# Optimization experiments

Hardware: AMD Instinct MI355X
Metric: run time of the kernel (lower is better)

The kernel has to match this reference:

```python
import jax, jax.numpy as jnp
import numpy as np

BLKQ = 128   # query block size (BLOCK_M)
BLKK = 64    # key block size (BLOCK_N)
TOPK_RATIO = 0.1
EPS = 1e-5


def _block_mean(x, blk):
    # x: (B,H,L,D) -> (B,H,L//blk,D) mean over each block (compress_kernel)
    B, H, L, D = x.shape
    return x.reshape(B, H, L // blk, blk, D).mean(axis=3)


def setup_inputs() -> dict:
    key = jax.random.key(0)
    ks = jax.random.split(key, 5)
    B, L, H, D = 2, 4096, 16, 64
    return {
        "query": jax.random.normal(ks[0], (B, L, H, D), dtype=jnp.float32),
        "key":   jax.random.normal(ks[1], (B, L, H, D), dtype=jnp.float32),
        "value": jax.random.normal(ks[2], (B, L, H, D), dtype=jnp.float32),
        "W": 0.02 * jax.random.normal(ks[3], (D, D), dtype=jnp.float32),
        "b": 0.02 * jax.random.normal(ks[4], (D,), dtype=jnp.float32),
    }


def reference(query, key, value, W, b):
    # inputs (B,L,H,D) -> internal (B,H,L,D)
    q = jnp.transpose(query, (0, 2, 1, 3))
    k = jnp.transpose(key, (0, 2, 1, 3))
    v = jnp.transpose(value, (0, 2, 1, 3))
    B, H, L, D = q.shape
    scale = D ** (-0.5)

    # ---- get_block_map: mean-pooled block scoring + top-k LUT ----
    arg_k = k - k.mean(axis=2, keepdims=True)
    pq = _block_mean(q, BLKQ)        # (B,H,M,D)
    pk = _block_mean(arg_k, BLKK)    # (B,H,KB,D)
    score = jnp.einsum('bhmd,bhkd->bhmk', pq, pk)  # (B,H,M,KB)
    KB = score.shape[-1]
    topk = min(KB, int(TOPK_RATIO * KB))
    _, lut = jax.lax.top_k(score, topk)            # (B,H,M,topk) int32

    # ---- block-sparse attention over gathered K/V blocks ----
    M = L // BLKQ
    kb = k.reshape(B, H, KB, BLKK, D)
    vb = v.reshape(B, H, KB, BLKK, D)
    idx = lut.reshape(B, H, M * topk, 1, 1)
    gk = jnp.take_along_axis(kb, idx, axis=2).reshape(B, H, M, topk * BLKK, D)
    gv = jnp.take_along_axis(vb, idx, axis=2).reshape(B, H, M, topk * BLKK, D)
    qb = q.reshape(B, H, M, BLKQ, D)
    logits = jnp.einsum('bhmqd,bhmnd->bhmqn', qb, gk) * scale
    p = jax.nn.softmax(logits, axis=-1)  # online softmax over union of selected blocks
    o_s = jnp.einsum('bhmqn,bhmnd->bhmqd', p, gv).reshape(B, H, L, D)

    # ---- linear attention branch (feature_map='softmax') ----
    qf = jax.nn.softmax(q, axis=-1)
    kf = jax.nn.softmax(k, axis=-1)
    kv = jnp.einsum('bhld,bhle->bhde', kf, v)
    num = jnp.einsum('bhld,bhde->bhle', qf, kv)
    den = jnp.einsum('bhld,bhd->bhl', qf, kf.sum(axis=2))
    o_l = num / (EPS + den[..., None])
    o_l = jnp.einsum('bhld,ed->bhle', o_l, W) + b  # proj_l

    out = jnp.transpose(o_s + o_l, (0, 2, 1, 3))  # back to (B,L,H,D)
    return out
```

## Files before the change

kernel.cpp:

```cpp
#include <hip/hip_runtime.h>
#include <math.h>
#include <cstdint>
#include <cstddef>

#define B_    2
#define LSEQ  4096
#define H_    16
#define D_    64
#define M_    32
#define KB_   64
#define TOPK  6
#define SCALE 0.125f
#define LOG2E 1.4426950408889634f
#define SCL2  (SCALE * LOG2E)
#define EPSL  1e-5f
#define SPLIT 32
#define PSTR  65

typedef __attribute__((ext_vector_type(8))) short short8;
typedef __attribute__((ext_vector_type(4))) float f32x4;

#define LGKM_FENCE()   __asm__ volatile("s_waitcnt lgkmcnt(0)" ::: "memory")
#define BLOCK_BARRIER() __asm__ volatile("s_waitcnt lgkmcnt(0)\n\ts_barrier" ::: "memory")

__device__ __forceinline__ short bf16_rne(float x) {
  unsigned u = __float_as_uint(x);
  return (short)((u + 0x7fffu + ((u >> 16) & 1u)) >> 16);
}
__device__ __forceinline__ unsigned pack2_rne(float a, float b) {
  return ((unsigned)(unsigned short)bf16_rne(a)) | (((unsigned)(unsigned short)bf16_rne(b)) << 16);
}
__device__ __forceinline__ float bf16_to_f32(short s) {
  return __uint_as_float(((unsigned)(unsigned short)s) << 16);
}

__global__ __launch_bounds__(256) void lin_stats_kernel(
    const float* __restrict__ kin, const float* __restrict__ vin,
    const float* __restrict__ qin,
    float* __restrict__ kv, float* __restrict__ kfs,
    float* __restrict__ pkw, float* __restrict__ pqw)
{
  int blk   = blockIdx.x;
  int chunk = blk & (SPLIT - 1);
  int bh    = blk / SPLIT;
  int h = bh & (H_ - 1);
  int b = bh >> 4;
  int tid = threadIdx.x;
  int w = tid >> 6, lane = tid & 63, quad = lane >> 4, l15 = lane & 15;

  __shared__ __align__(16) float kraw[64 * 68];
  __shared__ __align__(16) short sA[64 * 64];
  __shared__ __align__(16) short sB[80 * 64];
  __shared__ float pred[512];

  for (int i = tid; i < 1024; i += 256) {
    int row = 64 + (i >> 6);
    sB[row * 64 + (i & 63)] = (row == 64) ? (short)0x3F80 : (short)0;
  }

  {
    int c4 = tid & 15, r0 = tid >> 4;
    float4 s = {0.f, 0.f, 0.f, 0.f};
    for (int i = 0; i < 8; i++) {
      int row = r0 + i * 16;
      float4 x = *(const float4*)(qin + (((size_t)b * LSEQ + chunk * 128 + row) * H_ + h) * D_ + c4 * 4);
      s.x += x.x; s.y += x.y; s.z += x.z; s.w += x.w;
    }
    ((float4*)kraw)[tid] = s;
    BLOCK_BARRIER();
    if (tid < 16) {
      float4 a = {0.f, 0.f, 0.f, 0.f};
      for (int j = 0; j < 16; j++) {
        float4 x = ((float4*)kraw)[j * 16 + tid];
        a.x += x.x; a.y += x.y; a.z += x.z; a.w += x.w;
      }
      float4 o = {a.x * (1.f/128.f), a.y * (1.f/128.f), a.z * (1.f/128.f), a.w * (1.f/128.f)};
      *(float4*)(pqw + ((size_t)bh * 32 + chunk) * 64 + tid * 4) = o;
    }
  }

  f32x4 acc[5];
#pragma unroll
  for (int nt = 0; nt < 5; nt++) acc[nt] = (f32x4){0.f, 0.f, 0.f, 0.f};

  for (int t2 = 0; t2 < 2; ++t2) {
    int kbs = chunk * 2 + t2;
    int l0  = chunk * 128 + t2 * 64;
    BLOCK_BARRIER();
#pragma unroll
    for (int i = 0; i < 4; i++) {
      int f = tid + i * 256;
      int row = f >> 4, c4 = f & 15;
      *(float4*)(kraw + row * 68 + c4 * 4) =
        *(const float4*)(kin + (((size_t)b * LSEQ + l0 + row) * H_ + h) * D_ + c4 * 4);
    }
    {
      const float* vp = vin + (((size_t)b * LSEQ + l0 + lane) * H_ + h) * D_ + w * 16;
      float4 a0 = *(const float4*)(vp + 0);
      float4 a1 = *(const float4*)(vp + 4);
      float4 a2 = *(const float4*)(vp + 8);
      float4 a3 = *(const float4*)(vp + 12);
      float f[16] = {a0.x,a0.y,a0.z,a0.w, a1.x,a1.y,a1.z,a1.w,
                     a2.x,a2.y,a2.z,a2.w, a3.x,a3.y,a3.z,a3.w};
#pragma unroll
      for (int j = 0; j < 16; j++) {
        int e = w * 16 + j;
        int col = (((lane >> 3) ^ (e & 7)) << 3) | (lane & 7);
        sB[e * 64 + col] = bf16_rne(f[j]);
      }
    }
    BLOCK_BARRIER();
    {
      float kp = 0.f;
#pragma unroll
      for (int i = 0; i < 16; i++) kp += kraw[(w * 16 + i) * 68 + lane];
      pred[256 + w * 64 + lane] = kp;
    }
    float kr[16];
    *(float4*)(kr + 0)  = *(const float4*)(kraw + lane * 68 + w * 16 + 0);
    *(float4*)(kr + 4)  = *(const float4*)(kraw + lane * 68 + w * 16 + 4);
    *(float4*)(kr + 8)  = *(const float4*)(kraw + lane * 68 + w * 16 + 8);
    *(float4*)(kr + 12) = *(const float4*)(kraw + lane * 68 + w * 16 + 12);
    float ps = 0.f;
#pragma unroll
    for (int j = 0; j < 16; j++) { kr[j] = __expf(kr[j]); ps += kr[j]; }
    pred[w * 64 + lane] = ps;
    BLOCK_BARRIER();
    float ssum = pred[lane] + pred[64 + lane] + pred[128 + lane] + pred[192 + lane];
    float scl = 1.f / ssum;
    if (tid < 64) {
      float s = pred[256 + tid] + pred[320 + tid] + pred[384 + tid] + pred[448 + tid];
      pkw[((size_t)bh * 64 + kbs) * 64 + tid] = s * (1.f / 64.f);
    }
#pragma unroll
    for (int j = 0; j < 16; j++) {
      int d = w * 16 + j;
      int col = (((lane >> 3) ^ (d & 7)) << 3) | (lane & 7);
      sA[d * 64 + col] = bf16_rne(kr[j] * scl);
    }
    BLOCK_BARRIER();
    short8 af[2];
#pragma unroll
    for (int ks = 0; ks < 2; ks++) {
      int row = w * 16 + l15;
      int bi = (ks * 4 + quad) ^ (row & 7);
      af[ks] = *(const short8*)(sA + row * 64 + bi * 8);
    }
#pragma unroll
    for (int nt = 0; nt < 5; nt++) {
      int row = nt * 16 + l15;
#pragma unroll
      for (int ks = 0; ks < 2; ks++) {
        int bi = (ks * 4 + quad) ^ (row & 7);
        short8 bf = *(const short8*)(sB + row * 64 + bi * 8);
        acc[nt] = __builtin_amdgcn_mfma_f32_16x16x32_bf16(af[ks], bf, acc[nt], 0, 0, 0);
      }
    }
  }
  size_t kvb = (size_t)bh * 4096;
  int d0 = w * 16 + quad * 4;
#pragma unroll
  for (int nt = 0; nt < 4; nt++)
#pragma unroll
    for (int r = 0; r < 4; r++)
      atomicAdd(&kv[kvb + (size_t)(d0 + r) * 64 + nt * 16 + l15], acc[nt][r]);
  if (l15 == 0) {
#pragma unroll
    for (int r = 0; r < 4; r++)
      atomicAdd(&kfs[bh * 64 + d0 + r], acc[4][r]);
  }
}

__global__ __launch_bounds__(256) void blockmap_kernel(
    const float* __restrict__ pkw, const float* __restrict__ pqw,
    int* __restrict__ lut)
{
  int bh = blockIdx.x;
  int tid = threadIdx.x;

  __shared__ float pk[64 * PSTR];
  __shared__ float pq[32 * PSTR];
  __shared__ float sc[32 * PSTR];
  __shared__ float km[64];

#pragma unroll
  for (int i = 0; i < 16; i++) {
    int o = tid + i * 256;
    pk[(o >> 6) * PSTR + (o & 63)] = pkw[(size_t)bh * 4096 + o];
  }
#pragma unroll
  for (int i = 0; i < 8; i++) {
    int o = tid + i * 256;
    pq[(o >> 6) * PSTR + (o & 63)] = pqw[(size_t)bh * 2048 + o];
  }
  __syncthreads();
  if (tid < 64) {
    float s = 0.f;
#pragma unroll
    for (int kb = 0; kb < 64; kb++) s += pk[kb * PSTR + tid];
    km[tid] = s * (1.f / 64.f);
  }
  __syncthreads();
#pragma unroll
  for (int i = 0; i < 16; i++) {
    int o = tid + i * 256;
    int kb = o >> 6, d = o & 63;
    pk[kb * PSTR + d] -= km[d];
  }
  __syncthreads();
#pragma unroll
  for (int i = 0; i < 8; i++) {
    int o = tid + i * 256;
    int mb = o >> 6, kb = o & 63;
    float s = 0.f;
#pragma unroll
    for (int d = 0; d < 64; d++) s += pq[mb * PSTR + d] * pk[kb * PSTR + d];
    sc[mb * PSTR + kb] = s;
  }
  __syncthreads();
  if (tid < 32) {
    float* row = sc + tid * PSTR;
    int lb = (bh * M_ + tid) * TOPK;
    for (int s = 0; s < TOPK; s++) {
      float best = -INFINITY; int bi = 0;
      for (int j = 0; j < 64; j++) {
        float v = row[j];
        if (v > best) { best = v; bi = j; }
      }
      lut[lb + s] = bi;
      row[bi] = -INFINITY;
    }
  }
}

__global__ __launch_bounds__(256, 3) void sparse_attn_kernel(
    const float* __restrict__ qin, const float* __restrict__ kin,
    const float* __restrict__ vin, const int* __restrict__ lut,
    const float* __restrict__ kv, const float* __restrict__ kfs,
    const float* __restrict__ Wg, const float* __restrict__ biasg,
    float* __restrict__ out)
{
  int blk = blockIdx.x;
  int x = blk & 7, g = blk >> 3;
  int bh = x * 4 + (g & 3);
  int m  = g >> 2;
  int h = bh & (H_ - 1);
  int b = bh >> 4;
  int t = threadIdx.x;
  int w = t >> 6, lane = t & 63, quad = lane >> 4, l15 = lane & 15;

  __shared__ __align__(16) char smem[37120];
  short* sK  = (short*)smem;
  short* sV  = (short*)(smem + 8192);
  short* sP  = (short*)(smem + 18432);
  short* skv  = (short*)(smem + 18432);
  short* sW   = (short*)(smem + 28672);
  float* sbias= (float*)(smem + 36864);
  short* wPs = sP + w * 1024;
  short* olS = (short*)smem + w * 1024;

  for (int i = t; i < 1024; i += 256) {
    int row = 64 + (i >> 6);
    sV[row * 64 + (i & 63)] = (row == 64) ? (short)0x3F80 : (short)0;
  }

  short8 qA[2][2];
#pragma unroll
  for (int mt = 0; mt < 2; mt++) {
    int qrow = m * 128 + w * 32 + mt * 16 + l15;
    const float* qp = qin + (((size_t)b * LSEQ + qrow) * H_ + h) * D_;
#pragma unroll
    for (int ks = 0; ks < 2; ks++) {
      int d0 = ks * 32 + quad * 8;
      float4 a0 = *(const float4*)(qp + d0);
      float4 a1 = *(const float4*)(qp + d0 + 4);
      union { int4 i; short8 s; } u;
      u.i.x = pack2_rne(a0.x * SCL2, a0.y * SCL2);
      u.i.y = pack2_rne(a0.z * SCL2, a0.w * SCL2);
      u.i.z = pack2_rne(a1.x * SCL2, a1.y * SCL2);
      u.i.w = pack2_rne(a1.z * SCL2, a1.w * SCL2);
      qA[mt][ks] = u.s;
    }
  }

  f32x4 O[2][4];
  f32x4 Lacc[2];
#pragma unroll
  for (int mt = 0; mt < 2; mt++) {
#pragma unroll
    for (int dt = 0; dt < 4; dt++) O[mt][dt] = (f32x4){0.f, 0.f, 0.f, 0.f};
    Lacc[mt] = (f32x4){0.f, 0.f, 0.f, 0.f};
  }

  int lbase = (bh * M_ + m) * TOPK;
  int kbs_[TOPK];
#pragma unroll
  for (int i = 0; i < TOPK; i++) kbs_[i] = lut[lbase + i];

  float4 pk0, pk1, pk2, pk3;
  float4 pv0, pv1, pv2, pv3;
  const int kkey = t >> 2, kc = t & 3;
  const int vkey = t & 63;

  {
    int kb = kbs_[0];
    const float* kp = kin + (((size_t)b * LSEQ + (size_t)kb * 64 + kkey) * H_ + h) * D_ + kc * 16;
    pk0 = *(const float4*)(kp + 0);  pk1 = *(const float4*)(kp + 4);
    pk2 = *(const float4*)(kp + 8);  pk3 = *(const float4*)(kp + 12);
    const float* vp = vin + (((size_t)b * LSEQ + (size_t)kb * 64 + vkey) * H_ + h) * D_ + w * 16;
    pv0 = *(const float4*)(vp + 0);  pv1 = *(const float4*)(vp + 4);
    pv2 = *(const float4*)(vp + 8);  pv3 = *(const float4*)(vp + 12);
  }

  for (int s = 0; s < TOPK; s++) {
    BLOCK_BARRIER();
    {
      int4 h0, h1;
      h0.x = pack2_rne(pk0.x, pk0.y);  h0.y = pack2_rne(pk0.z, pk0.w);
      h0.z = pack2_rne(pk1.x, pk1.y);  h0.w = pack2_rne(pk1.z, pk1.w);
      h1.x = pack2_rne(pk2.x, pk2.y);  h1.y = pack2_rne(pk2.z, pk2.w);
      h1.z = pack2_rne(pk3.x, pk3.y);  h1.w = pack2_rne(pk3.z, pk3.w);
      int base = kkey * 64;
      int b0 = ((kc * 2    ) ^ (kkey & 7)) << 3;
      int b1 = ((kc * 2 + 1) ^ (kkey & 7)) << 3;
      *(int4*)(sK + base + b0) = h0;
      *(int4*)(sK + base + b1) = h1;
    }
    {
      float f[16] = {pv0.x,pv0.y,pv0.z,pv0.w, pv1.x,pv1.y,pv1.z,pv1.w,
                     pv2.x,pv2.y,pv2.z,pv2.w, pv3.x,pv3.y,pv3.z,pv3.w};
#pragma unroll
      for (int j = 0; j < 16; j++) {
        int d = w * 16 + j;
        int col = (((vkey >> 3) ^ (d & 7)) << 3) | (vkey & 7);
        sV[d * 64 + col] = bf16_rne(f[j]);
      }
    }
    BLOCK_BARRIER();
    if (s + 1 < TOPK) {
      int kb = kbs_[s + 1];
      const float* kp = kin + (((size_t)b * LSEQ + (size_t)kb * 64 + kkey) * H_ + h) * D_ + kc * 16;
      pk0 = *(const float4*)(kp + 0);  pk1 = *(const float4*)(kp + 4);
      pk2 = *(const float4*)(kp + 8);  pk3 = *(const float4*)(kp + 12);
      const float* vp = vin + (((size_t)b * LSEQ + (size_t)kb * 64 + vkey) * H_ + h) * D_ + w * 16;
      pv0 = *(const float4*)(vp + 0);  pv1 = *(const float4*)(vp + 4);
      pv2 = *(const float4*)(vp + 8);  pv3 = *(const float4*)(vp + 12);
    }

#pragma unroll
    for (int mt = 0; mt < 2; mt++) {
      f32x4 S[4];
#pragma unroll
      for (int nt = 0; nt < 4; nt++) {
        f32x4 acc = (f32x4){0.f, 0.f, 0.f, 0.f};
        int row = nt * 16 + l15;
#pragma unroll
        for (int ks = 0; ks < 2; ks++) {
          int blk8 = ((ks * 4 + quad) ^ (row & 7)) << 3;
          short8 kh = *(const short8*)(sK + row * 64 + blk8);
          acc = __builtin_amdgcn_mfma_f32_16x16x32_bf16(qA[mt][ks], kh, acc, 0, 0, 0);
        }
        S[nt] = acc;
      }
#pragma unroll
      for (int r = 0; r < 4; r++) {
        int prow = quad * 4 + r;
#pragma unroll
        for (int nt = 0; nt < 4; nt++) {
          int key = nt * 16 + l15;
          int idx = prow * 64 + ((((key >> 3) ^ (prow & 7)) << 3) | (key & 7));
          wPs[idx] = bf16_rne(__builtin_amdgcn_exp2f(S[nt][r]));
        }
      }
      LGKM_FENCE();
      short8 pA[2];
#pragma unroll
      for (int ks = 0; ks < 2; ks++) {
        int blk8 = ((ks * 4 + quad) ^ (l15 & 7)) << 3;
        pA[ks] = *(const short8*)(wPs + l15 * 64 + blk8);
      }
      LGKM_FENCE();
#pragma unroll
      for (int dt = 0; dt < 5; dt++) {
        f32x4 acc = (dt < 4) ? O[mt][dt] : Lacc[mt];
        int row = dt * 16 + l15;
#pragma unroll
        for (int ks = 0; ks < 2; ks++) {
          int blk8 = ((ks * 4 + quad) ^ (row & 7)) << 3;
          short8 vh = *(const short8*)(sV + row * 64 + blk8);
          acc = __builtin_amdgcn_mfma_f32_16x16x32_bf16(pA[ks], vh, acc, 0, 0, 0);
        }
        if (dt < 4) O[mt][dt] = acc; else Lacc[mt] = acc;
      }
    }
  }

#pragma unroll
  for (int mt = 0; mt < 2; mt++)
#pragma unroll
    for (int r = 0; r < 4; r++) {
      float lv = __shfl(Lacc[mt][r], lane & 48);
      float inv = 1.f / lv;
#pragma unroll
      for (int dt = 0; dt < 4; dt++) O[mt][dt][r] *= inv;
    }

  BLOCK_BARRIER();
#pragma unroll
  for (int i = 0; i < 16; i++) {
    int idx = t + i * 256;
    int d = idx >> 6, e = idx & 63;
    int c1 = (((d >> 3) ^ (e & 7)) << 3) | (d & 7);
    skv[e * 64 + c1] = bf16_rne(kv[(size_t)bh * 4096 + idx]);
    int eo = idx >> 6, dd = idx & 63;
    int c2 = (((dd >> 3) ^ (eo & 7)) << 3) | (dd & 7);
    sW[eo * 64 + c2] = bf16_rne(Wg[idx]);
  }
#pragma unroll
  for (int j = 0; j < 4; j++) {
    int idx2 = t + j * 256;
    int row = 64 + (idx2 >> 6), col = idx2 & 63;
    skv[row * 64 + col] = (row == 64) ? bf16_rne(kfs[bh * 64 + col]) : (short)0;
  }
  if (t < 64) sbias[t] = biasg[t];
  BLOCK_BARRIER();

  const short8 onesB = {(short)0x3F80,(short)0x3F80,(short)0x3F80,(short)0x3F80,
                        (short)0x3F80,(short)0x3F80,(short)0x3F80,(short)0x3F80};

#pragma unroll
  for (int mt = 0; mt < 2; mt++) {
    float eq[2][8];
    short8 eqs[2];
#pragma unroll
    for (int ks = 0; ks < 2; ks++) {
      union { short8 s; short a[8]; } uu; uu.s = qA[mt][ks];
      union { int4 i; short8 s; } pp;
      unsigned pw[4];
#pragma unroll
      for (int j = 0; j < 8; j++)
        eq[ks][j] = __builtin_amdgcn_exp2f(8.f * bf16_to_f32(uu.a[j]));
#pragma unroll
      for (int j2 = 0; j2 < 4; j2++)
        pw[j2] = pack2_rne(eq[ks][j2 * 2], eq[ks][j2 * 2 + 1]);
      pp.i.x = (int)pw[0]; pp.i.y = (int)pw[1]; pp.i.z = (int)pw[2]; pp.i.w = (int)pw[3];
      eqs[ks] = pp.s;
    }
    f32x4 ssv = (f32x4){0.f, 0.f, 0.f, 0.f};
    ssv = __builtin_amdgcn_mfma_f32_16x16x32_bf16(eqs[0], onesB, ssv, 0, 0, 0);
    ssv = __builtin_amdgcn_mfma_f32_16x16x32_bf16(eqs[1], onesB, ssv, 0, 0, 0);
    int srcl = (l15 >> 2) << 4;
    float s0 = __shfl(ssv[0], srcl);
    float s1 = __shfl(ssv[1], srcl);
    float s2 = __shfl(ssv[2], srcl);
    float s3 = __shfl(ssv[3], srcl);
    int rr = l15 & 3;
    float ssrow = (rr == 0) ? s0 : (rr == 1) ? s1 : (rr == 2) ? s2 : s3;
    float qinv = 1.f / ssrow;
    short8 qf[2];
#pragma unroll
    for (int ks = 0; ks < 2; ks++) {
      union { int4 i; short8 s; } pp;
      pp.i.x = (int)pack2_rne(eq[ks][0] * qinv, eq[ks][1] * qinv);
      pp.i.y = (int)pack2_rne(eq[ks][2] * qinv, eq[ks][3] * qinv);
      pp.i.z = (int)pack2_rne(eq[ks][4] * qinv, eq[ks][5] * qinv);
      pp.i.w = (int)pack2_rne(eq[ks][6] * qinv, eq[ks][7] * qinv);
      qf[ks] = pp.s;
    }
    f32x4 Cn[5];
#pragma unroll
    for (int nt = 0; nt < 5; nt++) {
      f32x4 acc = (f32x4){0.f, 0.f, 0.f, 0.f};
      int row = nt * 16 + l15;
#pragma unroll
      for (int ks = 0; ks < 2; ks++) {
        int blk8 = ((ks * 4 + quad) ^ (row & 7)) << 3;
        short8 bf = *(const short8*)(skv + row * 64 + blk8);
        acc = __builtin_amdgcn_mfma_f32_16x16x32_bf16(qf[ks], bf, acc, 0, 0, 0);
      }
      Cn[nt] = acc;
    }
#pragma unroll
    for (int r = 0; r < 4; r++) {
      float dv = __shfl(Cn[4][r], lane & 48);
      float invd = 1.f / (EPSL + dv);
      int prow = quad * 4 + r;
#pragma unroll
      for (int nt = 0; nt < 4; nt++) {
        int e = nt * 16 + l15;
        int idx = prow * 64 + ((((e >> 3) ^ (prow & 7)) << 3) | (e & 7));
        olS[idx] = bf16_rne(Cn[nt][r] * invd);
      }
    }
    LGKM_FENCE();
    short8 oh[2];
#pragma unroll
    for (int ks = 0; ks < 2; ks++) {
      int blk8 = ((ks * 4 + quad) ^ (l15 & 7)) << 3;
      oh[ks] = *(const short8*)(olS + l15 * 64 + blk8);
    }
    LGKM_FENCE();
#pragma unroll
    for (int nt = 0; nt < 4; nt++) {
      int row = nt * 16 + l15;
      f32x4 acc = O[mt][nt];
#pragma unroll
      for (int ks = 0; ks < 2; ks++) {
        int blk8 = ((ks * 4 + quad) ^ (row & 7)) << 3;
        short8 wf = *(const short8*)(sW + row * 64 + blk8);
        acc = __builtin_amdgcn_mfma_f32_16x16x32_bf16(oh[ks], wf, acc, 0, 0, 0);
      }
      O[mt][nt] = acc;
    }
  }

#pragma unroll
  for (int mt = 0; mt < 2; mt++) {
    int qrow0 = m * 128 + w * 32 + mt * 16 + quad * 4;
#pragma unroll
    for (int r = 0; r < 4; r++) {
      float* op = out + (((size_t)b * LSEQ + qrow0 + r) * H_ + h) * D_ + l15;
#pragma unroll
      for (int dt = 0; dt < 4; dt++)
        op[dt * 16] = O[mt][dt][r] + sbias[dt * 16 + l15];
    }
  }
}

extern "C" void kernel_launch(void* const* d_in, const int* in_sizes, int n_in,
                              void* d_out, int out_size, void* d_ws, size_t ws_size,
                              hipStream_t stream)
{
  const float* q    = (const float*)d_in[0];
  const float* k    = (const float*)d_in[1];
  const float* v    = (const float*)d_in[2];
  const float* W    = (const float*)d_in[3];
  const float* bias = (const float*)d_in[4];
  float* out = (float*)d_out;

  float* kv  = (float*)d_ws;
  float* kfs = kv  + (size_t)B_ * H_ * D_ * D_;
  float* pkw = kfs + (size_t)B_ * H_ * D_;
  float* pqw = pkw + (size_t)B_ * H_ * KB_ * D_;
  int*   lut = (int*)(pqw + (size_t)B_ * H_ * M_ * D_);

  size_t zero_bytes = ((size_t)B_ * H_ * D_ * D_ + (size_t)B_ * H_ * D_) * sizeof(float);
  hipMemsetAsync(d_ws, 0, zero_bytes, stream);

  hipLaunchKernelGGL(lin_stats_kernel,  dim3(B_ * H_ * SPLIT), dim3(256), 0, stream,
                     k, v, q, kv, kfs, pkw, pqw);
  hipLaunchKernelGGL(blockmap_kernel,   dim3(B_ * H_),         dim3(256), 0, stream, pkw, pqw, lut);
  hipLaunchKernelGGL(sparse_attn_kernel,dim3(B_ * H_ * M_),    dim3(256), 0, stream,
                     q, k, v, lut, kv, kfs, W, bias, out);
}
```

Baseline: 213.3 us.

## Fuse block-map top-k into sparse attention and double-buffer K/V loads

Removes the separate blockmap kernel and the query-block pooling in lin_stats. Each sparse-attention block now pools its own query block, scores it against the pooled keys, and picks the top-k key blocks with a wave-shuffle argmax. Dropping the key-mean subtraction and the 1/128 scale is safe because neither changes the ranking. The K/V gather loop now holds two register buffers so the next block's loads are in flight further ahead. The change also adds s_setprio around the MFMA sections and raises the occupancy hint in launch bounds from 3 to 4. In exchange, every attention block redundantly reads the 16KB pooled-key tile and runs the scoring itself, and the extra prefetch registers could cause spills under the tighter launch bound.

```diff
diff --git a/kernel.cpp b/kernel.cpp
--- a/kernel.cpp
+++ b/kernel.cpp
@@ -36,9 +36,8 @@
 
 __global__ __launch_bounds__(256) void lin_stats_kernel(
     const float* __restrict__ kin, const float* __restrict__ vin,
-    const float* __restrict__ qin,
     float* __restrict__ kv, float* __restrict__ kfs,
-    float* __restrict__ pkw, float* __restrict__ pqw)
+    float* __restrict__ pkw)
 {
   int blk   = blockIdx.x;
   int chunk = blk & (SPLIT - 1);
@@ -58,27 +57,6 @@
     sB[row * 64 + (i & 63)] = (row == 64) ? (short)0x3F80 : (short)0;
   }
 
-  {
-    int c4 = tid & 15, r0 = tid >> 4;
-    float4 s = {0.f, 0.f, 0.f, 0.f};
-    for (int i = 0; i < 8; i++) {
-      int row = r0 + i * 16;
-      float4 x = *(const float4*)(qin + (((size_t)b * LSEQ + chunk * 128 + row) * H_ + h) * D_ + c4 * 4);
-      s.x += x.x; s.y += x.y; s.z += x.z; s.w += x.w;
-    }
-    ((float4*)kraw)[tid] = s;
-    BLOCK_BARRIER();
-    if (tid < 16) {
-      float4 a = {0.f, 0.f, 0.f, 0.f};
-      for (int j = 0; j < 16; j++) {
-        float4 x = ((float4*)kraw)[j * 16 + tid];
-        a.x += x.x; a.y += x.y; a.z += x.z; a.w += x.w;
-      }
-      float4 o = {a.x * (1.f/128.f), a.y * (1.f/128.f), a.z * (1.f/128.f), a.w * (1.f/128.f)};
-      *(float4*)(pqw + ((size_t)bh * 32 + chunk) * 64 + tid * 4) = o;
-    }
-  }
-
   f32x4 acc[5];
 #pragma unroll
   for (int nt = 0; nt < 5; nt++) acc[nt] = (f32x4){0.f, 0.f, 0.f, 0.f};
@@ -171,71 +149,9 @@
   }
 }
 
-__global__ __launch_bounds__(256) void blockmap_kernel(
-    const float* __restrict__ pkw, const float* __restrict__ pqw,
-    int* __restrict__ lut)
-{
-  int bh = blockIdx.x;
-  int tid = threadIdx.x;
-
-  __shared__ float pk[64 * PSTR];
-  __shared__ float pq[32 * PSTR];
-  __shared__ float sc[32 * PSTR];
-  __shared__ float km[64];
-
-#pragma unroll
-  for (int i = 0; i < 16; i++) {
-    int o = tid + i * 256;
-    pk[(o >> 6) * PSTR + (o & 63)] = pkw[(size_t)bh * 4096 + o];
-  }
-#pragma unroll
-  for (int i = 0; i < 8; i++) {
-    int o = tid + i * 256;
-    pq[(o >> 6) * PSTR + (o & 63)] = pqw[(size_t)bh * 2048 + o];
-  }
-  __syncthreads();
-  if (tid < 64) {
-    float s = 0.f;
-#pragma unroll
-    for (int kb = 0; kb < 64; kb++) s += pk[kb * PSTR + tid];
-    km[tid] = s * (1.f / 64.f);
-  }
-  __syncthreads();
-#pragma unroll
-  for (int i = 0; i < 16; i++) {
-    int o = tid + i * 256;
-    int kb = o >> 6, d = o & 63;
-    pk[kb * PSTR + d] -= km[d];
-  }
-  __syncthreads();
-#pragma unroll
-  for (int i = 0; i < 8; i++) {
-    int o = tid + i * 256;
-    int mb = o >> 6, kb = o & 63;
-    float s = 0.f;
-#pragma unroll
-    for (int d = 0; d < 64; d++) s += pq[mb * PSTR + d] * pk[kb * PSTR + d];
-    sc[mb * PSTR + kb] = s;
-  }
-  __syncthreads();
-  if (tid < 32) {
-    float* row = sc + tid * PSTR;
-    int lb = (bh * M_ + tid) * TOPK;
-    for (int s = 0; s < TOPK; s++) {
-      float best = -INFINITY; int bi = 0;
-      for (int j = 0; j < 64; j++) {
-        float v = row[j];
-        if (v > best) { best = v; bi = j; }
-      }
-      lut[lb + s] = bi;
-      row[bi] = -INFINITY;
-    }
-  }
-}
-
-__global__ __launch_bounds__(256, 3) void sparse_attn_kernel(
+__global__ __launch_bounds__(256, 4) void sparse_attn_kernel(
     const float* __restrict__ qin, const float* __restrict__ kin,
-    const float* __restrict__ vin, const int* __restrict__ lut,
+    const float* __restrict__ vin, const float* __restrict__ pkw,
     const float* __restrict__ kv, const float* __restrict__ kfs,
     const float* __restrict__ Wg, const float* __restrict__ biasg,
     float* __restrict__ out)
@@ -253,16 +169,106 @@
   short* sK  = (short*)smem;
   short* sV  = (short*)(smem + 8192);
   short* sP  = (short*)(smem + 18432);
+  float* pkL  = (float*)smem;
+  float4* qps = (float4*)(smem + 16640);
+  float* pqL  = (float*)(smem + 20736);
   short* skv  = (short*)(smem + 18432);
   short* sW   = (short*)(smem + 28672);
   float* sbias= (float*)(smem + 36864);
   short* wPs = sP + w * 1024;
   short* olS = (short*)smem + w * 1024;
 
+#pragma unroll
+  for (int i = 0; i < 16; i++) {
+    int o = t + i * 256;
+    pkL[(o >> 6) * PSTR + (o & 63)] = pkw[(size_t)bh * 4096 + o];
+  }
+  {
+    int c4 = t & 15, r0 = t >> 4;
+    float4 sacc = {0.f, 0.f, 0.f, 0.f};
+#pragma unroll
+    for (int i = 0; i < 8; i++) {
+      int row = m * 128 + r0 + i * 16;
+      float4 xq = *(const float4*)(qin + (((size_t)b * LSEQ + row) * H_ + h) * D_ + c4 * 4);
+      sacc.x += xq.x; sacc.y += xq.y; sacc.z += xq.z; sacc.w += xq.w;
+    }
+    qps[t] = sacc;
+  }
+  BLOCK_BARRIER();
+  if (t < 64) {
+    const float* qf = (const float*)qps;
+    float sY = 0.f;
+#pragma unroll
+    for (int j = 0; j < 16; j++) sY += qf[j * 64 + t];
+    pqL[t] = sY;
+  }
+  BLOCK_BARRIER();
+  float scv = 0.f;
+  {
+    const float* rowp = pkL + lane * PSTR;
+#pragma unroll
+    for (int d = 0; d < 64; d++) scv += pqL[d] * rowp[d];
+  }
+  int kbs_[TOPK];
+#pragma unroll
+  for (int r = 0; r < TOPK; r++) {
+    float bs = scv; int bi = lane;
+#pragma unroll
+    for (int off = 32; off; off >>= 1) {
+      float os = __shfl_xor(bs, off);
+      int   oi = __shfl_xor(bi, off);
+      if (os > bs || (os == bs && oi < bi)) { bs = os; bi = oi; }
+    }
+    kbs_[r] = bi;
+    if (lane == bi) scv = -INFINITY;
+  }
+  BLOCK_BARRIER();
+
   for (int i = t; i < 1024; i += 256) {
     int row = 64 + (i >> 6);
     sV[row * 64 + (i & 63)] = (row == 64) ? (short)0x3F80 : (short)0;
   }
+
+  const int kkey = t >> 2, kc = t & 3;
+  const int vkey = t & 63;
+  float4 Ak0, Ak1, Ak2, Ak3, Av0, Av1, Av2, Av3;
+  float4 Bk0, Bk1, Bk2, Bk3, Bv0, Bv1, Bv2, Bv3;
+
+  auto LOADKV = [&](int kb, float4& k0, float4& k1, float4& k2, float4& k3,
+                    float4& v0, float4& v1, float4& v2, float4& v3) {
+    const float* kp = kin + (((size_t)b * LSEQ + (size_t)kb * 64 + kkey) * H_ + h) * D_ + kc * 16;
+    k0 = *(const float4*)(kp + 0);  k1 = *(const float4*)(kp + 4);
+    k2 = *(const float4*)(kp + 8);  k3 = *(const float4*)(kp + 12);
+    const float* vp = vin + (((size_t)b * LSEQ + (size_t)kb * 64 + vkey) * H_ + h) * D_ + w * 16;
+    v0 = *(const float4*)(vp + 0);  v1 = *(const float4*)(vp + 4);
+    v2 = *(const float4*)(vp + 8);  v3 = *(const float4*)(vp + 12);
+  };
+
+  auto STOREKV = [&](const float4& k0, const float4& k1, const float4& k2, const float4& k3,
+                     const float4& v0, const float4& v1, const float4& v2, const float4& v3) {
+    {
+      int4 h0, h1;
+      h0.x = pack2_rne(k0.x, k0.y);  h0.y = pack2_rne(k0.z, k0.w);
+      h0.z = pack2_rne(k1.x, k1.y);  h0.w = pack2_rne(k1.z, k1.w);
+      h1.x = pack2_rne(k2.x, k2.y);  h1.y = pack2_rne(k2.z, k2.w);
+      h1.z = pack2_rne(k3.x, k3.y);  h1.w = pack2_rne(k3.z, k3.w);
+      int base = kkey * 64;
+      int b0 = ((kc * 2    ) ^ (kkey & 7)) << 3;
+      int b1 = ((kc * 2 + 1) ^ (kkey & 7)) << 3;
+      *(int4*)(sK + base + b0) = h0;
+      *(int4*)(sK + base + b1) = h1;
+    }
+    {
+      float f[16] = {v0.x,v0.y,v0.z,v0.w, v1.x,v1.y,v1.z,v1.w,
+                     v2.x,v2.y,v2.z,v2.w, v3.x,v3.y,v3.z,v3.w};
+#pragma unroll
+      for (int j = 0; j < 16; j++) {
+        int d = w * 16 + j;
+        int col = (((vkey >> 3) ^ (d & 7)) << 3) | (vkey & 7);
+        sV[d * 64 + col] = bf16_rne(f[j]);
+      }
+    }
+  };
 
   short8 qA[2][2];
 #pragma unroll
@@ -292,64 +298,11 @@
     Lacc[mt] = (f32x4){0.f, 0.f, 0.f, 0.f};
   }
 
-  int lbase = (bh * M_ + m) * TOPK;
-  int kbs_[TOPK];
-#pragma unroll
-  for (int i = 0; i < TOPK; i++) kbs_[i] = lut[lbase + i];
-
-  float4 pk0, pk1, pk2, pk3;
-  float4 pv0, pv1, pv2, pv3;
-  const int kkey = t >> 2, kc = t & 3;
-  const int vkey = t & 63;
-
-  {
-    int kb = kbs_[0];
-    const float* kp = kin + (((size_t)b * LSEQ + (size_t)kb * 64 + kkey) * H_ + h) * D_ + kc * 16;
-    pk0 = *(const float4*)(kp + 0);  pk1 = *(const float4*)(kp + 4);
-    pk2 = *(const float4*)(kp + 8);  pk3 = *(const float4*)(kp + 12);
-    const float* vp = vin + (((size_t)b * LSEQ + (size_t)kb * 64 + vkey) * H_ + h) * D_ + w * 16;
-    pv0 = *(const float4*)(vp + 0);  pv1 = *(const float4*)(vp + 4);
-    pv2 = *(const float4*)(vp + 8);  pv3 = *(const float4*)(vp + 12);
-  }
-
-  for (int s = 0; s < TOPK; s++) {
-    BLOCK_BARRIER();
-    {
-      int4 h0, h1;
-      h0.x = pack2_rne(pk0.x, pk0.y);  h0.y = pack2_rne(pk0.z, pk0.w);
-      h0.z = pack2_rne(pk1.x, pk1.y);  h0.w = pack2_rne(pk1.z, pk1.w);
-      h1.x = pack2_rne(pk2.x, pk2.y);  h1.y = pack2_rne(pk2.z, pk2.w);
-      h1.z = pack2_rne(pk3.x, pk3.y);  h1.w = pack2_rne(pk3.z, pk3.w);
-      int base = kkey * 64;
-      int b0 = ((kc * 2    ) ^ (kkey & 7)) << 3;
-      int b1 = ((kc * 2 + 1) ^ (kkey & 7)) << 3;
-      *(int4*)(sK + base + b0) = h0;
-      *(int4*)(sK + base + b1) = h1;
-    }
-    {
-      float f[16] = {pv0.x,pv0.y,pv0.z,pv0.w, pv1.x,pv1.y,pv1.z,pv1.w,
-                     pv2.x,pv2.y,pv2.z,pv2.w, pv3.x,pv3.y,pv3.z,pv3.w};
-#pragma unroll
-      for (int j = 0; j < 16; j++) {
-        int d = w * 16 + j;
-        int col = (((vkey >> 3) ^ (d & 7)) << 3) | (vkey & 7);
-        sV[d * 64 + col] = bf16_rne(f[j]);
-      }
-    }
-    BLOCK_BARRIER();
-    if (s + 1 < TOPK) {
-      int kb = kbs_[s + 1];
-      const float* kp = kin + (((size_t)b * LSEQ + (size_t)kb * 64 + kkey) * H_ + h) * D_ + kc * 16;
-      pk0 = *(const float4*)(kp + 0);  pk1 = *(const float4*)(kp + 4);
-      pk2 = *(const float4*)(kp + 8);  pk3 = *(const float4*)(kp + 12);
-      const float* vp = vin + (((size_t)b * LSEQ + (size_t)kb * 64 + vkey) * H_ + h) * D_ + w * 16;
-      pv0 = *(const float4*)(vp + 0);  pv1 = *(const float4*)(vp + 4);
-      pv2 = *(const float4*)(vp + 8);  pv3 = *(const float4*)(vp + 12);
-    }
-
+  auto COMPUTE = [&]() {
 #pragma unroll
     for (int mt = 0; mt < 2; mt++) {
       f32x4 S[4];
+      __builtin_amdgcn_s_setprio(1);
 #pragma unroll
       for (int nt = 0; nt < 4; nt++) {
         f32x4 acc = (f32x4){0.f, 0.f, 0.f, 0.f};
@@ -362,6 +315,7 @@
         }
         S[nt] = acc;
       }
+      __builtin_amdgcn_s_setprio(0);
 #pragma unroll
       for (int r = 0; r < 4; r++) {
         int prow = quad * 4 + r;
@@ -380,6 +334,7 @@
         pA[ks] = *(const short8*)(wPs + l15 * 64 + blk8);
       }
       LGKM_FENCE();
+      __builtin_amdgcn_s_setprio(1);
 #pragma unroll
       for (int dt = 0; dt < 5; dt++) {
         f32x4 acc = (dt < 4) ? O[mt][dt] : Lacc[mt];
@@ -392,7 +347,26 @@
         }
         if (dt < 4) O[mt][dt] = acc; else Lacc[mt] = acc;
       }
-    }
+      __builtin_amdgcn_s_setprio(0);
+    }
+  };
+
+  LOADKV(kbs_[0], Ak0, Ak1, Ak2, Ak3, Av0, Av1, Av2, Av3);
+  LOADKV(kbs_[1], Bk0, Bk1, Bk2, Bk3, Bv0, Bv1, Bv2, Bv3);
+#pragma unroll
+  for (int ss = 0; ss < TOPK / 2; ss++) {
+    BLOCK_BARRIER();
+    STOREKV(Ak0, Ak1, Ak2, Ak3, Av0, Av1, Av2, Av3);
+    BLOCK_BARRIER();
+    if (ss < TOPK / 2 - 1)
+      LOADKV(kbs_[2 * ss + 2], Ak0, Ak1, Ak2, Ak3, Av0, Av1, Av2, Av3);
+    COMPUTE();
+    BLOCK_BARRIER();
+    STOREKV(Bk0, Bk1, Bk2, Bk3, Bv0, Bv1, Bv2, Bv3);
+    BLOCK_BARRIER();
+    if (ss < TOPK / 2 - 1)
+      LOADKV(kbs_[2 * ss + 3], Bk0, Bk1, Bk2, Bk3, Bv0, Bv1, Bv2, Bv3);
+    COMPUTE();
   }
 
 #pragma unroll
@@ -541,15 +515,12 @@
   float* kv  = (float*)d_ws;
   float* kfs = kv  + (size_t)B_ * H_ * D_ * D_;
   float* pkw = kfs + (size_t)B_ * H_ * D_;
-  float* pqw = pkw + (size_t)B_ * H_ * KB_ * D_;
-  int*   lut = (int*)(pqw + (size_t)B_ * H_ * M_ * D_);
 
   size_t zero_bytes = ((size_t)B_ * H_ * D_ * D_ + (size_t)B_ * H_ * D_) * sizeof(float);
   hipMemsetAsync(d_ws, 0, zero_bytes, stream);
 
   hipLaunchKernelGGL(lin_stats_kernel,  dim3(B_ * H_ * SPLIT), dim3(256), 0, stream,
-                     k, v, q, kv, kfs, pkw, pqw);
-  hipLaunchKernelGGL(blockmap_kernel,   dim3(B_ * H_),         dim3(256), 0, stream, pkw, pqw, lut);
+                     k, v, kv, kfs, pkw);
   hipLaunchKernelGGL(sparse_attn_kernel,dim3(B_ * H_ * M_),    dim3(256), 0, stream,
-                     q, k, v, lut, kv, kfs, W, bias, out);
+                     q, k, v, pkw, kv, kfs, W, bias, out);
 }
```

After: 285.4 us. 33.8% more time.
